# Performance work log

Hardware: AMD Instinct MI355X
Metric: run time of the kernel (lower is better)

## Reference

```python
import jax, jax.numpy as jnp
import numpy as np

N, E, L, F, M = 512, 2048, 16, 16, 8
HOPS = 2      # egonet radius (k_hop_subgraph num_hops)
H = 128       # WL hash buckets
N_ITER = 3    # WeisfeilerLehman(n_iter=3)
TAU = 0.1     # soft-relabeling temperature


def setup_inputs():
    key = jax.random.key(0)
    k0, k1, k2, k3, k4, k5 = jax.random.split(key, 6)
    labels = jax.random.randint(k0, (N,), 0, L)
    x = jax.nn.one_hot(labels, L, dtype=jnp.float32)
    edge_index = jax.random.randint(k1, (2, E), 0, N)
    # filter adjacencies, built exactly as in GKernel.__init__:
    # symmetric 0/1 with zero diagonal
    A = jax.random.uniform(k2, (F, M, M))
    A = ((A + jnp.swapaxes(A, -1, -2)) > 1.0).astype(jnp.float32)
    A = A * (1.0 - jnp.eye(M, dtype=jnp.float32))
    Xlab = jax.random.randint(k3, (F, M), 0, L)
    X = jax.nn.one_hot(Xlab, L, dtype=jnp.float32)
    # injective label -> bucket embedding (random distinct buckets)
    E0 = jax.nn.one_hot(jax.random.permutation(k4, H)[:L], H, dtype=jnp.float32)
    # random projection used to hash (own-label, neighbor-multiset) signatures
    Rproj = jax.random.normal(k5, (2 * H, H), dtype=jnp.float32)
    return {"x": x, "edge_index": edge_index, "P": A, "X": X, "E0": E0, "Rproj": Rproj}


def _wl_features(c0, nbr_sum, mask, Rproj):
    # soft Weisfeiler-Lehman subtree features: at each iteration the new
    # node label is a hash of (own label, neighbor-label multiset); the
    # graph feature is the concatenated per-iteration label histograms.
    c = c0 * mask[:, None]                       # [n, H]
    feats = [c.sum(0)]
    for _ in range(N_ITER):
        sig = jnp.concatenate([c, nbr_sum(c)], axis=-1)        # [n, 2H]
        c = jax.nn.softmax((sig @ Rproj) / TAU, axis=-1) * mask[:, None]
        feats.append(c.sum(0))
    return jnp.concatenate(feats)                # [(N_ITER+1)*H]


def _max_comp_mask(A):
    # largest connected component via min-label propagation (max_comp)
    comp = jnp.arange(M, dtype=jnp.float32)
    Ab = A > 0
    for _ in range(M):
        nbr_min = jnp.min(jnp.where(Ab, comp[None, :], 1e9), axis=1)
        comp = jnp.minimum(comp, nbr_min)
    ci = comp.astype(jnp.int32)
    counts = jax.ops.segment_sum(jnp.ones(M, jnp.float32), ci, num_segments=M)
    best = jnp.argmax(counts)
    return (ci == best).astype(jnp.float32)


def reference(x, edge_index, P, X, E0, Rproj):
    # symmetrize edges (egonets / WL kernels are undirected)
    src = jnp.concatenate([edge_index[0], edge_index[1]])
    dst = jnp.concatenate([edge_index[1], edge_index[0]])
    # --- k-hop egonet node masks (compute_egonets) : reach[i, j] = 1 iff
    # node j is within HOPS hops of root i ---
    reach = jnp.eye(N, dtype=jnp.float32)
    for _ in range(HOPS):
        agg = jax.ops.segment_sum(reach[:, src].T, dst, num_segments=N).T
        reach = jnp.clip(reach + agg, 0.0, 1.0)
    c0 = x @ E0                                  # initial bucket labels [N, H]

    def ego_feat(mask):
        emask = (mask[src] * mask[dst])[:, None]
        def nbr(c):
            return jax.ops.segment_sum(c[src] * emask, dst, num_segments=N)
        return _wl_features(c0, nbr, mask, Rproj)

    ego_feats = jax.vmap(ego_feat)(reach)        # [N, (N_ITER+1)*H]

    def filt_feat(Af, Xf):
        mask = _max_comp_mask(Af)
        Am = Af * mask[:, None] * mask[None, :]
        return _wl_features(Xf @ E0, lambda c: Am @ c, mask, Rproj)

    filt_feats = jax.vmap(filt_feat)(P, X)       # [F, (N_ITER+1)*H]

    # normalized WL kernel: k(g1,g2)/sqrt(k(g1,g1) k(g2,g2)); sim.T -> [N, F]
    sim = filt_feats @ ego_feats.T               # [F, N]
    nf = jnp.linalg.norm(filt_feats, axis=-1)
    ng = jnp.linalg.norm(ego_feats, axis=-1)
    sim = sim / (nf[:, None] * ng[None, :] + 1e-12)
    return sim.T
```

## Files before the change

### kernel.cpp

```cpp
#include <hip/hip_runtime.h>
#include <hip/hip_bf16.h>

#define NN 512
#define EE 2048
#define LL 16
#define FF 16
#define MM 8
#define HH 128
#define CAP_ROWS 40960
#define MAXD 32
#define TAU_SCALE 14.426950408889634f

typedef __attribute__((ext_vector_type(8))) short bf16x8;
typedef __attribute__((ext_vector_type(4))) float f32x4;

constexpr size_t OFF_ADJ   = 0;
constexpr size_t SZ_ADJ    = (size_t)NN * 8 * 8;
constexpr size_t OFF_DEG   = OFF_ADJ + SZ_ADJ;
constexpr size_t SZ_DEG    = (size_t)NN * 4;
constexpr size_t OFF_CNT   = OFF_DEG + SZ_DEG;
constexpr size_t SZ_CNT    = (size_t)NN * 4;
constexpr size_t OFF_ROFF  = OFF_CNT + SZ_CNT;
constexpr size_t SZ_ROFF   = (size_t)(NN + 1) * 4 + 12;
constexpr size_t OFF_BUCKN = OFF_ROFF + SZ_ROFF;
constexpr size_t SZ_BUCKN  = (size_t)NN * 4;
constexpr size_t OFF_BUCKF = OFF_BUCKN + SZ_BUCKN;
constexpr size_t SZ_BUCKF  = (size_t)FF * MM * 4;
constexpr size_t OFF_NLST  = ((OFF_BUCKF + SZ_BUCKF + 63) / 64) * 64;
constexpr size_t SZ_NLST   = (size_t)NN * MAXD * 2;
constexpr size_t OFF_CEGO  = OFF_NLST + SZ_NLST;
constexpr size_t SZ_CEGO   = (size_t)CAP_ROWS * 2;
constexpr size_t OFF_NCNT  = OFF_CEGO + SZ_CEGO;
constexpr size_t SZ_NCNT   = (size_t)CAP_ROWS * 2;
constexpr size_t OFF_RBK   = OFF_NCNT + SZ_NCNT;
constexpr size_t SZ_RBK    = (size_t)CAP_ROWS * 2;
constexpr size_t OFF_NBR   = OFF_RBK + SZ_RBK;
constexpr size_t SZ_NBR    = (size_t)CAP_ROWS * MAXD * 2;
constexpr size_t OFF_NBK   = OFF_NBR + SZ_NBR;
constexpr size_t SZ_NBK    = (size_t)CAP_ROWS * MAXD * 2;
constexpr size_t OFF_EGOF  = ((OFF_NBK + SZ_NBK + 63) / 64) * 64;
constexpr size_t SZ_EGOF   = (size_t)NN * 512 * 4;
constexpr size_t OFF_FILTF = OFF_EGOF + SZ_EGOF;
constexpr size_t SZ_FILTF  = (size_t)FF * 512 * 4;
constexpr size_t OFF_FNORM = OFF_FILTF + SZ_FILTF;
constexpr size_t SZ_FNORM  = 64;
constexpr size_t OFF_CA    = ((OFF_FNORM + SZ_FNORM + 255) / 256) * 256;
constexpr size_t SZ_CBUF   = (size_t)CAP_ROWS * HH * 4;
constexpr size_t OFF_CB    = OFF_CA + SZ_CBUF;

__device__ __forceinline__ unsigned f2bfbits(float x) {
    unsigned u = __float_as_uint(x);
    return (u + 0x7fffu + ((u >> 16) & 1u)) >> 16;
}
__device__ __forceinline__ float bf2f(unsigned hb) { return __uint_as_float(hb << 16); }

__global__ __launch_bounds__(256) void k_build(const int* __restrict__ ei,
                                               const float* __restrict__ x,
                                               const float* __restrict__ X,
                                               const float* __restrict__ E0,
                                               int* __restrict__ degN,
                                               unsigned short* __restrict__ nbrLstN,
                                               unsigned long long* __restrict__ adj,
                                               int* __restrict__ buckN,
                                               int* __restrict__ buckF) {
    int idx = blockIdx.x * blockDim.x + threadIdx.x;
    if (idx < EE) {
        int a = ei[idx], b = ei[EE + idx];
        int p = atomicAdd(&degN[a], 1);
        if (p < MAXD) nbrLstN[(size_t)a * MAXD + p] = (unsigned short)b;
        int q = atomicAdd(&degN[b], 1);
        if (q < MAXD) nbrLstN[(size_t)b * MAXD + q] = (unsigned short)a;
        atomicOr(&adj[(size_t)a * 8 + (b >> 6)], 1ull << (b & 63));
        atomicOr(&adj[(size_t)b * 8 + (a >> 6)], 1ull << (a & 63));
    } else if (idx < EE + NN) {
        int i = idx - EE;
        int lab = 0;
        for (int l = 0; l < LL; ++l) if (x[i * LL + l] > 0.5f) lab = l;
        int b = 0;
        for (int h = 0; h < HH; ++h) if (E0[lab * HH + h] > 0.5f) b = h;
        buckN[i] = b;
    } else if (idx < EE + NN + FF * MM) {
        int fm = idx - EE - NN;
        int lab = 0;
        for (int l = 0; l < LL; ++l) if (X[fm * LL + l] > 0.5f) lab = l;
        int b = 0;
        for (int h = 0; h < HH; ++h) if (E0[lab * HH + h] > 0.5f) b = h;
        buckF[fm] = b;
    }
}

__global__ __launch_bounds__(64) void k_reach(const unsigned long long* __restrict__ adj,
                                              unsigned long long* __restrict__ bitsR,
                                              int* __restrict__ count) {
    __shared__ unsigned long long r1[8];
    __shared__ unsigned long long r2[8];
    int i = blockIdx.x, t = threadIdx.x;
    if (t < 8) {
        unsigned long long v = adj[(size_t)i * 8 + t];
        if (t == (i >> 6)) v |= 1ull << (i & 63);
        r1[t] = v;
        r2[t] = v;
    }
    __syncthreads();
    unsigned long long p[8] = {0, 0, 0, 0, 0, 0, 0, 0};
    for (int rep = 0; rep < 8; ++rep) {
        if ((r1[rep] >> t) & 1ull) {
            int j = t + rep * 64;
#pragma unroll
            for (int w = 0; w < 8; ++w) p[w] |= adj[(size_t)j * 8 + w];
        }
    }
#pragma unroll
    for (int w = 0; w < 8; ++w)
        if (p[w]) atomicOr(&r2[w], p[w]);
    __syncthreads();
    if (t < 8) bitsR[(size_t)i * 8 + t] = r2[t];
    if (t == 0) {
        int acc = 0;
        for (int w = 0; w < 8; ++w) acc += __popcll(r2[w]);
        count[i] = acc;
    }
}

__global__ __launch_bounds__(512) void k_scan(const int* __restrict__ in,
                                              int* __restrict__ out) {
    __shared__ int s[NN];
    int t = threadIdx.x;
    s[t] = in[t];
    __syncthreads();
    for (int d = 1; d < NN; d <<= 1) {
        int v = (t >= d) ? s[t - d] : 0;
        __syncthreads();
        s[t] += v;
        __syncthreads();
    }
    out[t + 1] = s[t];
    if (t == 0) out[0] = 0;
}

__global__ __launch_bounds__(64) void k_pack(const unsigned long long* __restrict__ bitsR,
                                             const int* __restrict__ count,
                                             const int* __restrict__ rowOff,
                                             const int* __restrict__ degN,
                                             const unsigned short* __restrict__ nbrLstN,
                                             const int* __restrict__ buckN,
                                             unsigned short* __restrict__ nbrRow,
                                             unsigned short* __restrict__ nbrBuck,
                                             unsigned short* __restrict__ nbrCnt,
                                             unsigned short* __restrict__ rowBuck,
                                             unsigned short* __restrict__ cegoG,
                                             float* __restrict__ egoF) {
    __shared__ unsigned long long bits[8];
    __shared__ int wpre[8];
    __shared__ unsigned short cmap_s[NN];
    __shared__ unsigned short nodes_s[NN];
    __shared__ float f0[HH];
    int i = blockIdx.x, t = threadIdx.x;
    if (t < 8) bits[t] = bitsR[(size_t)i * 8 + t];
    if (t < 64) { f0[t] = 0.0f; f0[t + 64] = 0.0f; }
    __syncthreads();
    if (t == 0) {
        int acc = 0;
        for (int w = 0; w < 8; ++w) { wpre[w] = acc; acc += __popcll(bits[w]); }
    }
    __syncthreads();
    int base = rowOff[i];
    int n = count[i];
    if (base >= CAP_ROWS) n = 0;
    else if (base + n > CAP_ROWS) n = CAP_ROWS - base;
    for (int rep = 0; rep < 8; ++rep) {
        int j = t + rep * 64;
        unsigned long long word = bits[rep];
        unsigned short v = 0xFFFFu;
        if ((word >> t) & 1ull) {
            int idx = wpre[rep] + __popcll(word & ((1ull << t) - 1ull));
            if (idx < n) { v = (unsigned short)idx; nodes_s[idx] = (unsigned short)j; }
        }
        cmap_s[j] = v;
    }
    for (int q = 256 + t; q < 512; q += 64) egoF[(size_t)i * 512 + q] = 0.0f;
    __syncthreads();
    for (int m = t; m < n; m += 64) {
        int j = nodes_s[m];
        int b = buckN[j];
        atomicAdd(&f0[b], 1.0f);
        size_t row = (size_t)(base + m);
        rowBuck[row] = (unsigned short)b;
        int dn = degN[j]; if (dn > MAXD) dn = MAXD;
        int cnt = 0;
        for (int e = 0; e < dn; ++e) {
            unsigned short nbNode = nbrLstN[(size_t)j * MAXD + e];
            unsigned short nr = cmap_s[nbNode];
            if (nr != 0xFFFFu && cnt < MAXD) {
                nbrRow[row * MAXD + cnt] = (unsigned short)(base + nr);
                nbrBuck[row * MAXD + cnt] = (unsigned short)buckN[nbNode];
                cnt++;
            }
        }
        nbrCnt[row] = (unsigned short)cnt;
        cegoG[row] = (unsigned short)i;
    }
    __syncthreads();
    if (t < 64) {
        egoF[(size_t)i * 512 + t] = f0[t];
        egoF[(size_t)i * 512 + t + 64] = f0[t + 64];
    }
}

__global__ __launch_bounds__(256) void k_iter1(const int* __restrict__ count,
                                               const int* __restrict__ rowOff,
                                               const unsigned short* __restrict__ rowBuck,
                                               const unsigned short* __restrict__ nbrBuck,
                                               const unsigned short* __restrict__ nbrCnt,
                                               const float* __restrict__ Rg,
                                               float* __restrict__ cOut,
                                               float* __restrict__ egoF) {
    __shared__ float fs[HH];
    int i = blockIdx.x, tid = threadIdx.x;
    int base = rowOff[i];
    int n = count[i];
    if (base >= CAP_ROWS) n = 0;
    else if (base + n > CAP_ROWS) n = CAP_ROWS - base;
    if (tid < HH) fs[tid] = 0.0f;
    __syncthreads();
    const float* Rb = Rg + (size_t)HH * HH;
    int col = (tid & 7) * 16;
    float facc[16];
#pragma unroll
    for (int q = 0; q < 16; ++q) facc[q] = 0.0f;
    for (int m = tid >> 3; m < n; m += 32) {
        int gr = base + m;
        float z[16];
        const float* rt = Rg + (size_t)rowBuck[gr] * HH + col;
#pragma unroll
        for (int q = 0; q < 4; ++q) *(float4*)&z[q * 4] = *(const float4*)&rt[q * 4];
        int cnt = nbrCnt[gr];
        const unsigned short* nk = &nbrBuck[(size_t)gr * MAXD];
        for (int e = 0; e < cnt; ++e) {
            const float* rb = Rb + (size_t)nk[e] * HH + col;
#pragma unroll
            for (int q = 0; q < 4; ++q) {
                float4 rv = *(const float4*)&rb[q * 4];
                z[q * 4 + 0] += rv.x; z[q * 4 + 1] += rv.y;
                z[q * 4 + 2] += rv.z; z[q * 4 + 3] += rv.w;
            }
        }
        float mx = z[0];
#pragma unroll
        for (int q = 1; q < 16; ++q) mx = fmaxf(mx, z[q]);
        for (int off = 4; off > 0; off >>= 1) mx = fmaxf(mx, __shfl_xor(mx, off));
        float s = 0.0f;
#pragma unroll
        for (int q = 0; q < 16; ++q) { z[q] = exp2f((z[q] - mx) * TAU_SCALE); s += z[q]; }
        for (int off = 4; off > 0; off >>= 1) s += __shfl_xor(s, off);
        float inv = 1.0f / s;
        float* crow = cOut + (size_t)gr * HH + col;
#pragma unroll
        for (int q = 0; q < 16; ++q) { z[q] *= inv; facc[q] += z[q]; }
#pragma unroll
        for (int q = 0; q < 4; ++q) *(float4*)&crow[q * 4] = *(const float4*)&z[q * 4];
    }
#pragma unroll
    for (int q = 0; q < 16; ++q) atomicAdd(&fs[col + q], facc[q]);
    __syncthreads();
    if (tid < HH) egoF[(size_t)i * 512 + HH + tid] = fs[tid];
}

__global__ __launch_bounds__(256) void k_prep(const float* __restrict__ Rg,
                                              short* __restrict__ RtH,
                                              short* __restrict__ RtL) {
    int idx = blockIdx.x * blockDim.x + threadIdx.x;
    int col = idx >> 5;
    int kc = (idx & 31) * 8;
    bf16x8 hv, lv;
#pragma unroll
    for (int j = 0; j < 8; ++j) {
        float xv = Rg[(size_t)(kc + j) * HH + col];
        unsigned hb = f2bfbits(xv);
        hv[j] = (short)hb;
        lv[j] = (short)f2bfbits(xv - bf2f(hb));
    }
    *(bf16x8*)&RtH[(size_t)col * 256 + kc] = hv;
    *(bf16x8*)&RtL[(size_t)col * 256 + kc] = lv;
}

__global__ __launch_bounds__(64) void k_iter(const float* __restrict__ cur,
                                             float* __restrict__ nxt,
                                             const short* __restrict__ RtH,
                                             const short* __restrict__ RtL,
                                             const int* __restrict__ rowOff,
                                             const unsigned short* __restrict__ nbrRow,
                                             const unsigned short* __restrict__ nbrCnt,
                                             const unsigned short* __restrict__ cegoG,
                                             float* __restrict__ egoF,
                                             int it) {
    int Rtot = rowOff[NN];
    if (Rtot > CAP_ROWS) Rtot = CAP_ROWS;
    int r0 = blockIdx.x * 16;
    if (r0 >= Rtot) return;
    int tid = threadIdx.x;
    int c16 = tid & 15, g = tid >> 4;
    int kb = g * 8;
    int grA = r0 + c16;
    if (grA >= Rtot) grA = Rtot - 1;

    float ua[4][8];
#pragma unroll
    for (int s = 0; s < 4; ++s)
#pragma unroll
        for (int j = 0; j < 8; ++j) ua[s][j] = 0.0f;
    {
        int cnt = nbrCnt[grA];
        const unsigned short* nb = &nbrRow[(size_t)grA * MAXD];
        for (int e = 0; e < cnt; ++e) {
            const float* cr = &cur[(size_t)nb[e] * HH + kb];
#pragma unroll
            for (int s = 0; s < 4; ++s) {
                float4 v0 = *(const float4*)&cr[s * 32];
                float4 v1 = *(const float4*)&cr[s * 32 + 4];
                ua[s][0] += v0.x; ua[s][1] += v0.y; ua[s][2] += v0.z; ua[s][3] += v0.w;
                ua[s][4] += v1.x; ua[s][5] += v1.y; ua[s][6] += v1.z; ua[s][7] += v1.w;
            }
        }
    }

    f32x4 acc[8];
#pragma unroll
    for (int n = 0; n < 8; ++n) acc[n] = (f32x4)(0.0f);
    const short* bbH = RtH + (size_t)c16 * 256 + kb;
    const short* bbL = RtL + (size_t)c16 * 256 + kb;

#pragma unroll
    for (int s = 0; s < 4; ++s) {
        bf16x8 ahi, alo;
#pragma unroll
        for (int j = 0; j < 8; ++j) {
            float xv = ua[s][j];
            unsigned hb = f2bfbits(xv);
            ahi[j] = (short)hb;
            alo[j] = (short)f2bfbits(xv - bf2f(hb));
        }
        const int t = s + 4;
#pragma unroll
        for (int n = 0; n < 8; ++n) {
            bf16x8 bh = *(const bf16x8*)&bbH[n * 4096 + t * 32];
            bf16x8 bl = *(const bf16x8*)&bbL[n * 4096 + t * 32];
            acc[n] = __builtin_amdgcn_mfma_f32_16x16x32_bf16(ahi, bh, acc[n], 0, 0, 0);
            acc[n] = __builtin_amdgcn_mfma_f32_16x16x32_bf16(ahi, bl, acc[n], 0, 0, 0);
            acc[n] = __builtin_amdgcn_mfma_f32_16x16x32_bf16(alo, bh, acc[n], 0, 0, 0);
        }
    }
    {
        const float* cr = &cur[(size_t)grA * HH + kb];
#pragma unroll
        for (int t = 0; t < 4; ++t) {
            float4 v0 = *(const float4*)&cr[t * 32];
            float4 v1 = *(const float4*)&cr[t * 32 + 4];
            float cv[8] = {v0.x, v0.y, v0.z, v0.w, v1.x, v1.y, v1.z, v1.w};
            bf16x8 ahi, alo;
#pragma unroll
            for (int j = 0; j < 8; ++j) {
                unsigned hb = f2bfbits(cv[j]);
                ahi[j] = (short)hb;
                alo[j] = (short)f2bfbits(cv[j] - bf2f(hb));
            }
#pragma unroll
            for (int n = 0; n < 8; ++n) {
                bf16x8 bh = *(const bf16x8*)&bbH[n * 4096 + t * 32];
                bf16x8 bl = *(const bf16x8*)&bbL[n * 4096 + t * 32];
                acc[n] = __builtin_amdgcn_mfma_f32_16x16x32_bf16(ahi, bh, acc[n], 0, 0, 0);
                acc[n] = __builtin_amdgcn_mfma_f32_16x16x32_bf16(ahi, bl, acc[n], 0, 0, 0);
                acc[n] = __builtin_amdgcn_mfma_f32_16x16x32_bf16(alo, bh, acc[n], 0, 0, 0);
            }
        }
    }

    float inv[4];
#pragma unroll
    for (int i = 0; i < 4; ++i) {
        float m = acc[0][i];
#pragma unroll
        for (int n = 1; n < 8; ++n) m = fmaxf(m, acc[n][i]);
        for (int off = 8; off > 0; off >>= 1) m = fmaxf(m, __shfl_xor(m, off));
        float s = 0.0f;
#pragma unroll
        for (int n = 0; n < 8; ++n) {
            float e = exp2f((acc[n][i] - m) * TAU_SCALE);
            acc[n][i] = e; s += e;
        }
        for (int off = 8; off > 0; off >>= 1) s += __shfl_xor(s, off);
        inv[i] = 1.0f / s;
    }

    float fa[8];
#pragma unroll
    for (int n = 0; n < 8; ++n) fa[n] = 0.0f;
    int cege = -1;
#pragma unroll
    for (int i = 0; i < 4; ++i) {
        int gr = r0 + g * 4 + i;
        if (gr < Rtot) {
#pragma unroll
            for (int n = 0; n < 8; ++n) {
                float c = acc[n][i] * inv[i];
                nxt[(size_t)gr * HH + n * 16 + c16] = c;
                acc[n][i] = c;
            }
            int ego = cegoG[gr];
            if (ego != cege) {
                if (cege >= 0) {
#pragma unroll
                    for (int n = 0; n < 8; ++n) {
                        atomicAdd(&egoF[(size_t)cege * 512 + it * HH + n * 16 + c16], fa[n]);
                        fa[n] = 0.0f;
                    }
                }
                cege = ego;
            }
#pragma unroll
            for (int n = 0; n < 8; ++n) fa[n] += acc[n][i];
        }
    }
    if (cege >= 0) {
#pragma unroll
        for (int n = 0; n < 8; ++n)
            atomicAdd(&egoF[(size_t)cege * 512 + it * HH + n * 16 + c16], fa[n]);
    }
}

__global__ __launch_bounds__(256) void k_filt(const float* __restrict__ P,
                                              const int* __restrict__ buckF,
                                              const float* __restrict__ Rg,
                                              float* __restrict__ filtF,
                                              float* __restrict__ fnorm) {
    __shared__ float As[MM][MM];
    __shared__ float Am[MM][MM];
    __shared__ float msk[MM];
    __shared__ float cbuf[2][MM][HH];
    __shared__ float ubuf[MM][HH];
    __shared__ float feats[4 * HH];
    __shared__ float red4[4];
    int f = blockIdx.x, tid = threadIdx.x, wave = tid >> 6, lane = tid & 63;
    if (tid < 64) As[tid >> 3][tid & 7] = P[f * 64 + tid];
    for (int idx = tid; idx < 4 * HH; idx += 256) feats[idx] = 0.f;
    __syncthreads();
    if (tid == 0) {
        float comp[MM];
        for (int m = 0; m < MM; ++m) comp[m] = (float)m;
        for (int it = 0; it < MM; ++it) {
            float nm[MM];
            for (int j = 0; j < MM; ++j) {
                float mn = 1e9f;
                for (int k = 0; k < MM; ++k)
                    if (As[j][k] > 0.f) mn = fminf(mn, comp[k]);
                nm[j] = mn;
            }
            for (int j = 0; j < MM; ++j) comp[j] = fminf(comp[j], nm[j]);
        }
        int cnt[MM], ci[MM];
        for (int m = 0; m < MM; ++m) cnt[m] = 0;
        for (int m = 0; m < MM; ++m) { ci[m] = (int)comp[m]; cnt[ci[m]]++; }
        int best = 0;
        for (int m = 1; m < MM; ++m) if (cnt[m] > cnt[best]) best = m;
        for (int m = 0; m < MM; ++m) msk[m] = (ci[m] == best) ? 1.0f : 0.0f;
    }
    __syncthreads();
    if (tid < 64) Am[tid >> 3][tid & 7] = As[tid >> 3][tid & 7] * msk[tid >> 3] * msk[tid & 7];
    for (int idx = tid; idx < MM * HH; idx += 256) {
        int m = idx >> 7, h = idx & 127;
        cbuf[0][m][h] = (msk[m] > 0.f && h == buckF[f * MM + m]) ? 1.0f : 0.0f;
    }
    __syncthreads();
    if (tid < HH) {
        float s = 0.f;
        for (int m = 0; m < MM; ++m) s += cbuf[0][m][tid];
        feats[tid] = s;
    }
    __syncthreads();
    int cur = 0;
    int h2 = 2 * lane;
    for (int it = 1; it <= 3; ++it) {
#pragma unroll
        for (int jj = 0; jj < 2; ++jj) {
            int d = wave * 2 + jj;
            float u0 = 0.f, u1 = 0.f;
            for (int s = 0; s < MM; ++s) {
                float w = Am[d][s];
                u0 += w * cbuf[cur][s][h2];
                u1 += w * cbuf[cur][s][h2 + 1];
            }
            ubuf[d][h2] = u0;
            ubuf[d][h2 + 1] = u1;
        }
        float a0[2] = {0.f, 0.f}, a1[2] = {0.f, 0.f};
        for (int k = 0; k < HH; ++k) {
            float2 rt = *(const float2*)&Rg[(size_t)k * HH + h2];
            float2 rb = *(const float2*)&Rg[(size_t)(HH + k) * HH + h2];
#pragma unroll
            for (int jj = 0; jj < 2; ++jj) {
                int d = wave * 2 + jj;
                float cd = cbuf[cur][d][k];
                float ud = ubuf[d][k];
                a0[jj] += cd * rt.x + ud * rb.x;
                a1[jj] += cd * rt.y + ud * rb.y;
            }
        }
#pragma unroll
        for (int jj = 0; jj < 2; ++jj) {
            int d = wave * 2 + jj;
            float z0 = a0[jj], z1 = a1[jj];
            float m = fmaxf(z0, z1);
            for (int off = 32; off > 0; off >>= 1) m = fmaxf(m, __shfl_xor(m, off));
            float e0 = exp2f((z0 - m) * TAU_SCALE);
            float e1 = exp2f((z1 - m) * TAU_SCALE);
            float s = e0 + e1;
            for (int off = 32; off > 0; off >>= 1) s += __shfl_xor(s, off);
            float inv = msk[d] / s;
            float c0 = e0 * inv, c1 = e1 * inv;
            cbuf[1 - cur][d][h2] = c0;
            cbuf[1 - cur][d][h2 + 1] = c1;
            atomicAdd(&feats[it * HH + h2], c0);
            atomicAdd(&feats[it * HH + h2 + 1], c1);
        }
        __syncthreads();
        cur = 1 - cur;
    }
    float np = 0.f;
    for (int idx = tid; idx < 4 * HH; idx += 256) {
        float v = feats[idx];
        filtF[(size_t)f * 512 + idx] = v;
        np += v * v;
    }
    for (int off = 32; off > 0; off >>= 1) np += __shfl_xor(np, off);
    if (lane == 0) red4[wave] = np;
    __syncthreads();
    if (tid == 0) fnorm[f] = sqrtf(red4[0] + red4[1] + red4[2] + red4[3]);
}

__global__ __launch_bounds__(64) void k_sim(const float* __restrict__ egoF,
                                            const float* __restrict__ filtF,
                                            const float* __restrict__ fnorm,
                                            float* __restrict__ out) {
    int i = blockIdx.x, lane = threadIdx.x;
    float e[8];
    float ss = 0.f;
#pragma unroll
    for (int r = 0; r < 8; ++r) {
        e[r] = egoF[(size_t)i * 512 + r * 64 + lane];
        ss += e[r] * e[r];
    }
    for (int off = 32; off > 0; off >>= 1) ss += __shfl_xor(ss, off);
    float ng = sqrtf(ss);
    for (int f = 0; f < FF; ++f) {
        float d = 0.f;
#pragma unroll
        for (int r = 0; r < 8; ++r) d += e[r] * filtF[(size_t)f * 512 + r * 64 + lane];
        for (int off = 32; off > 0; off >>= 1) d += __shfl_xor(d, off);
        if (lane == 0) out[i * FF + f] = d / (fnorm[f] * ng + 1e-12f);
    }
}

extern "C" void kernel_launch(void* const* d_in, const int* in_sizes, int n_in,
                              void* d_out, int out_size, void* d_ws, size_t ws_size,
                              hipStream_t stream) {
    (void)in_sizes; (void)n_in; (void)out_size; (void)ws_size;
    const float* x  = (const float*)d_in[0];
    const int*   ei = (const int*)d_in[1];
    const float* P  = (const float*)d_in[2];
    const float* X  = (const float*)d_in[3];
    const float* E0 = (const float*)d_in[4];
    const float* Rg = (const float*)d_in[5];
    float* out = (float*)d_out;
    char* ws = (char*)d_ws;

    unsigned long long* adj   = (unsigned long long*)(ws + OFF_ADJ);
    int* degN   = (int*)(ws + OFF_DEG);
    int* count  = (int*)(ws + OFF_CNT);
    int* rowOff = (int*)(ws + OFF_ROFF);
    int* buckN  = (int*)(ws + OFF_BUCKN);
    int* buckF  = (int*)(ws + OFF_BUCKF);
    unsigned short* nbrLstN = (unsigned short*)(ws + OFF_NLST);
    unsigned short* cego    = (unsigned short*)(ws + OFF_CEGO);
    unsigned short* nbrCnt  = (unsigned short*)(ws + OFF_NCNT);
    unsigned short* rowBuck = (unsigned short*)(ws + OFF_RBK);
    unsigned short* nbrRow  = (unsigned short*)(ws + OFF_NBR);
    unsigned short* nbrBuck = (unsigned short*)(ws + OFF_NBK);
    float* egoF  = (float*)(ws + OFF_EGOF);
    float* filtF = (float*)(ws + OFF_FILTF);
    float* fnorm = (float*)(ws + OFF_FNORM);
    float* cA    = (float*)(ws + OFF_CA);
    float* cB    = (float*)(ws + OFF_CB);
    unsigned long long* bitsR = (unsigned long long*)(ws + OFF_CA);
    short* RtH = (short*)(ws + OFF_NBK);
    short* RtL = RtH + (size_t)HH * 256;

    hipMemsetAsync(ws, 0, OFF_CNT, stream);
    k_build<<<(EE + NN + FF * MM + 255) / 256, 256, 0, stream>>>(ei, x, X, E0, degN, nbrLstN,
                                                                 adj, buckN, buckF);
    k_reach<<<NN, 64, 0, stream>>>(adj, bitsR, count);
    k_scan<<<1, 512, 0, stream>>>(count, rowOff);
    k_pack<<<NN, 64, 0, stream>>>(bitsR, count, rowOff, degN, nbrLstN, buckN,
                                  nbrRow, nbrBuck, nbrCnt, rowBuck, cego, egoF);
    k_iter1<<<NN, 256, 0, stream>>>(count, rowOff, rowBuck, nbrBuck, nbrCnt, Rg, cB, egoF);
    k_prep<<<16, 256, 0, stream>>>(Rg, RtH, RtL);
    k_iter<<<CAP_ROWS / 16, 64, 0, stream>>>(cB, cA, RtH, RtL, rowOff, nbrRow, nbrCnt, cego, egoF, 2);
    k_iter<<<CAP_ROWS / 16, 64, 0, stream>>>(cA, cB, RtH, RtL, rowOff, nbrRow, nbrCnt, cego, egoF, 3);
    k_filt<<<FF, 256, 0, stream>>>(P, buckF, Rg, filtF, fnorm);
    k_sim<<<NN, 64, 0, stream>>>(egoF, filtF, fnorm, out);
}
```

Measured before the change: 305.7 us.

## Fold Rproj bf16 split into build kernel, swizzle blocks across XCDs, vectorize neighbor index loads

Moves the hi/lo bf16 transposition of Rproj into k_build, removing the separate k_prep launch, and gives the result its own workspace region. Both iteration kernels remap block IDs so consecutive blocks land on the same XCD, which should improve L2 locality. Neighbor index lists are now read eight at a time as one vector load, and k_iter loads the row's own features up front to overlap with the gather. The 8-wide index load reads past cnt into padded slots, and the swizzle assumes the grid size is a multiple of 8.

```diff
diff --git a/kernel.cpp b/kernel.cpp
--- a/kernel.cpp
+++ b/kernel.cpp
@@ -12,6 +12,7 @@
 #define TAU_SCALE 14.426950408889634f
 
 typedef __attribute__((ext_vector_type(8))) short bf16x8;
+typedef __attribute__((ext_vector_type(8))) unsigned short u16x8;
 typedef __attribute__((ext_vector_type(4))) float f32x4;
 
 constexpr size_t OFF_ADJ   = 0;
@@ -47,22 +48,31 @@
 constexpr size_t OFF_CA    = ((OFF_FNORM + SZ_FNORM + 255) / 256) * 256;
 constexpr size_t SZ_CBUF   = (size_t)CAP_ROWS * HH * 4;
 constexpr size_t OFF_CB    = OFF_CA + SZ_CBUF;
+constexpr size_t OFF_RT    = OFF_CB + SZ_CBUF;
 
 __device__ __forceinline__ unsigned f2bfbits(float x) {
     unsigned u = __float_as_uint(x);
     return (u + 0x7fffu + ((u >> 16) & 1u)) >> 16;
 }
 __device__ __forceinline__ float bf2f(unsigned hb) { return __uint_as_float(hb << 16); }
+
+__device__ __forceinline__ int xcd_swz(int bid, int nwg) {
+    int cpx = nwg >> 3;
+    return (bid & 7) * cpx + (bid >> 3);
+}
 
 __global__ __launch_bounds__(256) void k_build(const int* __restrict__ ei,
                                                const float* __restrict__ x,
                                                const float* __restrict__ X,
                                                const float* __restrict__ E0,
+                                               const float* __restrict__ Rg,
                                                int* __restrict__ degN,
                                                unsigned short* __restrict__ nbrLstN,
                                                unsigned long long* __restrict__ adj,
                                                int* __restrict__ buckN,
-                                               int* __restrict__ buckF) {
+                                               int* __restrict__ buckF,
+                                               short* __restrict__ RtH,
+                                               short* __restrict__ RtL) {
     int idx = blockIdx.x * blockDim.x + threadIdx.x;
     if (idx < EE) {
         int a = ei[idx], b = ei[EE + idx];
@@ -86,6 +96,20 @@
         int b = 0;
         for (int h = 0; h < HH; ++h) if (E0[lab * HH + h] > 0.5f) b = h;
         buckF[fm] = b;
+    } else if (idx < EE + NN + FF * MM + 4096) {
+        int pidx = idx - (EE + NN + FF * MM);
+        int col = pidx >> 5;
+        int kc = (pidx & 31) * 8;
+        bf16x8 hv, lv;
+#pragma unroll
+        for (int j = 0; j < 8; ++j) {
+            float xv = Rg[(size_t)(kc + j) * HH + col];
+            unsigned hb = f2bfbits(xv);
+            hv[j] = (short)hb;
+            lv[j] = (short)f2bfbits(xv - bf2f(hb));
+        }
+        *(bf16x8*)&RtH[(size_t)col * 256 + kc] = hv;
+        *(bf16x8*)&RtL[(size_t)col * 256 + kc] = lv;
     }
 }
 
@@ -216,7 +240,8 @@
                                                float* __restrict__ cOut,
                                                float* __restrict__ egoF) {
     __shared__ float fs[HH];
-    int i = blockIdx.x, tid = threadIdx.x;
+    int i = xcd_swz(blockIdx.x, NN);
+    int tid = threadIdx.x;
     int base = rowOff[i];
     int n = count[i];
     if (base >= CAP_ROWS) n = 0;
@@ -236,13 +261,19 @@
         for (int q = 0; q < 4; ++q) *(float4*)&z[q * 4] = *(const float4*)&rt[q * 4];
         int cnt = nbrCnt[gr];
         const unsigned short* nk = &nbrBuck[(size_t)gr * MAXD];
-        for (int e = 0; e < cnt; ++e) {
-            const float* rb = Rb + (size_t)nk[e] * HH + col;
-#pragma unroll
-            for (int q = 0; q < 4; ++q) {
-                float4 rv = *(const float4*)&rb[q * 4];
-                z[q * 4 + 0] += rv.x; z[q * 4 + 1] += rv.y;
-                z[q * 4 + 2] += rv.z; z[q * 4 + 3] += rv.w;
+        for (int eb = 0; eb < cnt; eb += 8) {
+            u16x8 nv = *(const u16x8*)&nk[eb];
+#pragma unroll
+            for (int j = 0; j < 8; ++j) {
+                if (eb + j < cnt) {
+                    const float* rb = Rb + (size_t)nv[j] * HH + col;
+#pragma unroll
+                    for (int q = 0; q < 4; ++q) {
+                        float4 rv = *(const float4*)&rb[q * 4];
+                        z[q * 4 + 0] += rv.x; z[q * 4 + 1] += rv.y;
+                        z[q * 4 + 2] += rv.z; z[q * 4 + 3] += rv.w;
+                    }
+                }
             }
         }
         float mx = z[0];
@@ -264,24 +295,6 @@
     for (int q = 0; q < 16; ++q) atomicAdd(&fs[col + q], facc[q]);
     __syncthreads();
     if (tid < HH) egoF[(size_t)i * 512 + HH + tid] = fs[tid];
-}
-
-__global__ __launch_bounds__(256) void k_prep(const float* __restrict__ Rg,
-                                              short* __restrict__ RtH,
-                                              short* __restrict__ RtL) {
-    int idx = blockIdx.x * blockDim.x + threadIdx.x;
-    int col = idx >> 5;
-    int kc = (idx & 31) * 8;
-    bf16x8 hv, lv;
-#pragma unroll
-    for (int j = 0; j < 8; ++j) {
-        float xv = Rg[(size_t)(kc + j) * HH + col];
-        unsigned hb = f2bfbits(xv);
-        hv[j] = (short)hb;
-        lv[j] = (short)f2bfbits(xv - bf2f(hb));
-    }
-    *(bf16x8*)&RtH[(size_t)col * 256 + kc] = hv;
-    *(bf16x8*)&RtL[(size_t)col * 256 + kc] = lv;
 }
 
 __global__ __launch_bounds__(64) void k_iter(const float* __restrict__ cur,
@@ -296,7 +309,7 @@
                                              int it) {
     int Rtot = rowOff[NN];
     if (Rtot > CAP_ROWS) Rtot = CAP_ROWS;
-    int r0 = blockIdx.x * 16;
+    int r0 = xcd_swz(blockIdx.x, gridDim.x) * 16;
     if (r0 >= Rtot) return;
     int tid = threadIdx.x;
     int c16 = tid & 15, g = tid >> 4;
@@ -304,6 +317,14 @@
     int grA = r0 + c16;
     if (grA >= Rtot) grA = Rtot - 1;
 
+    const float* crOwn = &cur[(size_t)grA * HH + kb];
+    float4 oc[8];
+#pragma unroll
+    for (int t = 0; t < 4; ++t) {
+        oc[2 * t]     = *(const float4*)&crOwn[t * 32];
+        oc[2 * t + 1] = *(const float4*)&crOwn[t * 32 + 4];
+    }
+
     float ua[4][8];
 #pragma unroll
     for (int s = 0; s < 4; ++s)
@@ -312,14 +333,20 @@
     {
         int cnt = nbrCnt[grA];
         const unsigned short* nb = &nbrRow[(size_t)grA * MAXD];
-        for (int e = 0; e < cnt; ++e) {
-            const float* cr = &cur[(size_t)nb[e] * HH + kb];
-#pragma unroll
-            for (int s = 0; s < 4; ++s) {
-                float4 v0 = *(const float4*)&cr[s * 32];
-                float4 v1 = *(const float4*)&cr[s * 32 + 4];
-                ua[s][0] += v0.x; ua[s][1] += v0.y; ua[s][2] += v0.z; ua[s][3] += v0.w;
-                ua[s][4] += v1.x; ua[s][5] += v1.y; ua[s][6] += v1.z; ua[s][7] += v1.w;
+        for (int eb = 0; eb < cnt; eb += 8) {
+            u16x8 nv = *(const u16x8*)&nb[eb];
+#pragma unroll
+            for (int j = 0; j < 8; ++j) {
+                if (eb + j < cnt) {
+                    const float* cr = &cur[(size_t)nv[j] * HH + kb];
+#pragma unroll
+                    for (int s = 0; s < 4; ++s) {
+                        float4 v0 = *(const float4*)&cr[s * 32];
+                        float4 v1 = *(const float4*)&cr[s * 32 + 4];
+                        ua[s][0] += v0.x; ua[s][1] += v0.y; ua[s][2] += v0.z; ua[s][3] += v0.w;
+                        ua[s][4] += v1.x; ua[s][5] += v1.y; ua[s][6] += v1.z; ua[s][7] += v1.w;
+                    }
+                }
             }
         }
     }
@@ -351,11 +378,10 @@
         }
     }
     {
-        const float* cr = &cur[(size_t)grA * HH + kb];
 #pragma unroll
         for (int t = 0; t < 4; ++t) {
-            float4 v0 = *(const float4*)&cr[t * 32];
-            float4 v1 = *(const float4*)&cr[t * 32 + 4];
+            float4 v0 = oc[2 * t];
+            float4 v1 = oc[2 * t + 1];
             float cv[8] = {v0.x, v0.y, v0.z, v0.w, v1.x, v1.y, v1.z, v1.w};
             bf16x8 ahi, alo;
 #pragma unroll
@@ -591,18 +617,17 @@
     float* cA    = (float*)(ws + OFF_CA);
     float* cB    = (float*)(ws + OFF_CB);
     unsigned long long* bitsR = (unsigned long long*)(ws + OFF_CA);
-    short* RtH = (short*)(ws + OFF_NBK);
+    short* RtH = (short*)(ws + OFF_RT);
     short* RtL = RtH + (size_t)HH * 256;
 
     hipMemsetAsync(ws, 0, OFF_CNT, stream);
-    k_build<<<(EE + NN + FF * MM + 255) / 256, 256, 0, stream>>>(ei, x, X, E0, degN, nbrLstN,
-                                                                 adj, buckN, buckF);
+    k_build<<<(EE + NN + FF * MM + 4096 + 255) / 256, 256, 0, stream>>>(
+        ei, x, X, E0, Rg, degN, nbrLstN, adj, buckN, buckF, RtH, RtL);
     k_reach<<<NN, 64, 0, stream>>>(adj, bitsR, count);
     k_scan<<<1, 512, 0, stream>>>(count, rowOff);
     k_pack<<<NN, 64, 0, stream>>>(bitsR, count, rowOff, degN, nbrLstN, buckN,
                                   nbrRow, nbrBuck, nbrCnt, rowBuck, cego, egoF);
     k_iter1<<<NN, 256, 0, stream>>>(count, rowOff, rowBuck, nbrBuck, nbrCnt, Rg, cB, egoF);
-    k_prep<<<16, 256, 0, stream>>>(Rg, RtH, RtL);
     k_iter<<<CAP_ROWS / 16, 64, 0, stream>>>(cB, cA, RtH, RtL, rowOff, nbrRow, nbrCnt, cego, egoF, 2);
     k_iter<<<CAP_ROWS / 16, 64, 0, stream>>>(cA, cB, RtH, RtL, rowOff, nbrRow, nbrCnt, cego, egoF, 3);
     k_filt<<<FF, 256, 0, stream>>>(P, buckF, Rg, filtF, fnorm);
```

New measurement: 308.9 us. About the same (+1.0%).
